# Kernel tuning notes

Measured on AMD Instinct MI355X. Metric: run time of the kernel, lower is better.

The kernel has to match this reference:

```python
import jax, jax.numpy as jnp
import numpy as np

N = 50000          # nodes
E = 1600000        # edges
H = 8              # heads
F = 16             # out feats per head (np1class)
IN = 256           # in feats
NEG_SLOPE = 0.2    # DGL GATConv default leaky_relu slope


def setup_inputs() -> dict:
    key = jax.random.key(0)
    ks = jax.random.split(key, 7)
    x = jax.random.normal(ks[0], (N, IN), dtype=jnp.float32)
    W = jax.random.normal(ks[1], (IN, H * F), dtype=jnp.float32) * 0.05
    attn_l = jax.random.normal(ks[2], (H, F), dtype=jnp.float32) * 0.05
    attn_r = jax.random.normal(ks[3], (H, F), dtype=jnp.float32) * 0.05
    bias = jax.random.normal(ks[4], (H * F,), dtype=jnp.float32) * 0.05
    src = jax.random.randint(ks[5], (E,), 0, N, dtype=jnp.int64)
    dst = jax.random.randint(ks[6], (E,), 0, N, dtype=jnp.int64)
    return {"x": x, "W": W, "attn_l": attn_l, "attn_r": attn_r,
            "bias": bias, "src": src, "dst": dst}


def reference(x, W, attn_l, attn_r, bias, src, dst):
    # Linear projection to heads: [N, H, F]
    feat = (x @ W).reshape(N, H, F)
    # Per-node attention halves: [N, H]
    el = jnp.einsum('nhf,hf->nh', feat, attn_l)
    er = jnp.einsum('nhf,hf->nh', feat, attn_r)
    # Edge scores: e = leaky_relu(el[src] + er[dst])  -> [E, H]
    e = jax.nn.leaky_relu(el[src] + er[dst], negative_slope=NEG_SLOPE)
    # Segment softmax over incoming edges of each destination node
    m = jax.ops.segment_max(e, dst, num_segments=N)           # [N, H]
    m = jnp.where(jnp.isfinite(m), m, 0.0)                    # empty segments
    m = jax.lax.stop_gradient(m)
    ex = jnp.exp(e - m[dst])                                  # [E, H]
    s = jax.ops.segment_sum(ex, dst, num_segments=N)          # [N, H]
    a = ex / jnp.maximum(s[dst], 1e-9)                        # [E, H]
    # Weighted aggregation of source features: [N, H, F]
    msg = a[:, :, None] * feat[src]
    rst = jax.ops.segment_sum(msg, dst, num_segments=N)
    rst = rst + bias.reshape(H, F)
    # Classifier: mean over heads -> [N, F]
    return rst.mean(axis=1)
```

## Files before the change

### kernel.cpp

```cpp
#include <hip/hip_runtime.h>
#include <hip/hip_bf16.h>

#define NH 8
#define NF 16
#define NIN 256
#define HF 128
#define BNODES 256
#define CAP 9216
#define BCH 4096

typedef __attribute__((ext_vector_type(8))) short bf16x8;
typedef __attribute__((ext_vector_type(4))) float f32x4;

__device__ __forceinline__ unsigned short f2bf(float f) {
    union { float f; unsigned int u; } v; v.f = f;
    unsigned int r = v.u + 0x7FFFu + ((v.u >> 16) & 1u);
    return (unsigned short)(r >> 16);
}
__device__ __forceinline__ float bf2f(unsigned short b) {
    union { unsigned int u; float f; } v; v.u = ((unsigned int)b) << 16;
    return v.f;
}

#define GROWS 128
__global__ __launch_bounds__(256) void gemm_mfma(const float* __restrict__ A,
                                                 const float* __restrict__ W,
                                                 const float* __restrict__ attn_l,
                                                 const float* __restrict__ attn_r,
                                                 unsigned short* __restrict__ featb,
                                                 float* __restrict__ el,
                                                 float* __restrict__ er, int M) {
    __shared__ unsigned short AsH[32][264];
    __shared__ unsigned short AsL[32][264];
    const int tid = threadIdx.x;
    const int wave = tid >> 6, lane = tid & 63;
    const int quad = lane >> 4, lq = lane & 15;
    const int row0 = blockIdx.x * GROWS;

    bf16x8 bfrag[8][2];
#pragma unroll
    for (int h2 = 0; h2 < 2; h2++) {
        const int col = (wave * 2 + h2) * 16 + lq;
#pragma unroll
        for (int kk = 0; kk < 8; kk++) {
            const int kb = kk * 32 + quad * 8;
            bf16x8 f;
#pragma unroll
            for (int j = 0; j < 8; j++)
                f[j] = (short)f2bf(W[(size_t)(kb + j) * HF + col]);
            bfrag[kk][h2] = f;
        }
    }
    const float al0 = attn_l[(wave * 2 + 0) * 16 + lq];
    const float al1 = attn_l[(wave * 2 + 1) * 16 + lq];
    const float ar0 = attn_r[(wave * 2 + 0) * 16 + lq];
    const float ar1 = attn_r[(wave * 2 + 1) * 16 + lq];

    const int srow = tid >> 3;

    for (int c = 0; c < 4; c++) {
        const int crow0 = row0 + c * 32;
        __syncthreads();
#pragma unroll
        for (int i = 0; i < 8; i++) {
            const int col = ((tid & 7) + i * 8) * 4;
            const int gr = crow0 + srow;
            float4 v = make_float4(0.f, 0.f, 0.f, 0.f);
            if (gr < M) v = *(const float4*)&A[(size_t)gr * NIN + col];
            const unsigned short h0 = f2bf(v.x), h1 = f2bf(v.y),
                                 h2b = f2bf(v.z), h3 = f2bf(v.w);
            *(ushort4*)&AsH[srow][col] = make_ushort4(h0, h1, h2b, h3);
            *(ushort4*)&AsL[srow][col] =
                make_ushort4(f2bf(v.x - bf2f(h0)), f2bf(v.y - bf2f(h1)),
                             f2bf(v.z - bf2f(h2b)), f2bf(v.w - bf2f(h3)));
        }
        __syncthreads();
#pragma unroll
        for (int s = 0; s < 2; s++) {
            f32x4 acc0 = {0.f, 0.f, 0.f, 0.f};
            f32x4 acc1 = {0.f, 0.f, 0.f, 0.f};
            const int ar = s * 16 + lq;
#pragma unroll
            for (int kk = 0; kk < 8; kk++) {
                const bf16x8 ah = *(const bf16x8*)&AsH[ar][kk * 32 + quad * 8];
                const bf16x8 al = *(const bf16x8*)&AsL[ar][kk * 32 + quad * 8];
                acc0 = __builtin_amdgcn_mfma_f32_16x16x32_bf16(ah, bfrag[kk][0], acc0, 0, 0, 0);
                acc1 = __builtin_amdgcn_mfma_f32_16x16x32_bf16(ah, bfrag[kk][1], acc1, 0, 0, 0);
                acc0 = __builtin_amdgcn_mfma_f32_16x16x32_bf16(al, bfrag[kk][0], acc0, 0, 0, 0);
                acc1 = __builtin_amdgcn_mfma_f32_16x16x32_bf16(al, bfrag[kk][1], acc1, 0, 0, 0);
            }
#pragma unroll
            for (int r = 0; r < 4; r++) {
                const int gr = crow0 + s * 16 + quad * 4 + r;
                float pl0 = acc0[r] * al0, pr0 = acc0[r] * ar0;
                float pl1 = acc1[r] * al1, pr1 = acc1[r] * ar1;
#pragma unroll
                for (int m = 1; m < 16; m <<= 1) {
                    pl0 += __shfl_xor(pl0, m, 64);
                    pr0 += __shfl_xor(pr0, m, 64);
                    pl1 += __shfl_xor(pl1, m, 64);
                    pr1 += __shfl_xor(pr1, m, 64);
                }
                if (gr < M) {
                    featb[(size_t)gr * HF + (wave * 2 + 0) * 16 + lq] = f2bf(acc0[r]);
                    featb[(size_t)gr * HF + (wave * 2 + 1) * 16 + lq] = f2bf(acc1[r]);
                    if (lq == 0) {
                        el[(size_t)gr * NH + wave * 2 + 0] = pl0;
                        el[(size_t)gr * NH + wave * 2 + 1] = pl1;
                        er[(size_t)gr * NH + wave * 2 + 0] = pr0;
                        er[(size_t)gr * NH + wave * 2 + 1] = pr1;
                    }
                }
            }
        }
    }
}

__global__ __launch_bounds__(256) void bin_kernel(const int* __restrict__ src,
                                                  const int* __restrict__ dst,
                                                  int* __restrict__ bcnt,
                                                  unsigned int* __restrict__ binned,
                                                  int E, int NB) {
    __shared__ unsigned int hist[256];
    __shared__ unsigned short lpos[BCH];
    const int tid = threadIdx.x;
    const int base = blockIdx.x * BCH;
    if (tid < NB) hist[tid] = 0;
    __syncthreads();
    const int cnt = min(BCH, E - base);
    for (int i = tid; i < cnt; i += 256) {
        const int b = dst[base + i] >> 8;
        lpos[i] = (unsigned short)atomicAdd(&hist[b], 1u);
    }
    __syncthreads();
    if (tid < NB) {
        const unsigned int c = hist[tid];
        if (c) hist[tid] = (unsigned int)(tid * CAP + atomicAdd(&bcnt[tid], (int)c));
    }
    __syncthreads();
    for (int i = tid; i < cnt; i += 256) {
        const int d = dst[base + i];
        const int b = d >> 8;
        const unsigned int pos = hist[b] + (unsigned int)lpos[i];
        binned[pos] = (unsigned int)src[base + i] | ((unsigned int)(d & 255) << 16);
    }
}

__global__ __launch_bounds__(256) void csr_kernel(const int* __restrict__ bcnt,
                                                  const unsigned int* __restrict__ binned,
                                                  int* __restrict__ nodeinfo,
                                                  unsigned short* __restrict__ srcsw,
                                                  int N) {
    __shared__ int len[BNODES], cur[BNODES];
    __shared__ int wsum[4];
    const int b = blockIdx.x, t = threadIdx.x;
    const int node0 = b << 8;
    const int cntb = bcnt[b];
    const unsigned int* bb = &binned[(size_t)b * CAP];
    unsigned short* sw = &srcsw[(size_t)b * CAP];
    len[t] = 0;
    __syncthreads();
    for (int i = t; i < cntb; i += 256) atomicAdd(&len[bb[i] >> 16], 1);
    __syncthreads();
    {
        const int lane = t & 63, w = t >> 6;
        const int v = len[t];
        int incl = v;
#pragma unroll
        for (int off = 1; off < 64; off <<= 1) {
            const int x = __shfl_up(incl, off, 64);
            if (lane >= off) incl += x;
        }
        if (lane == 63) wsum[w] = incl;
        __syncthreads();
        int wbase = 0;
        for (int k = 0; k < w; k++) wbase += wsum[k];
        const int excl = wbase + incl - v;
        cur[t] = excl;
        if (node0 + t < N) nodeinfo[node0 + t] = excl | (v << 16);
    }
    __syncthreads();
    for (int i = t; i < cntb; i += 256) {
        const unsigned int p = bb[i];
        const int pos = atomicAdd(&cur[p >> 16], 1);
        sw[pos] = (unsigned short)(p & 0xFFFFu);
    }
}

__global__ __launch_bounds__(128) void agg_kernel(const int* __restrict__ nodeinfo,
                                                  const unsigned short* __restrict__ srcsw,
                                                  const float* __restrict__ el,
                                                  const float* __restrict__ er,
                                                  const unsigned short* __restrict__ featb,
                                                  const float* __restrict__ bias,
                                                  float* __restrict__ out) {
    const int n = blockIdx.x;
    const int tid = threadIdx.x;
    __shared__ float lds_sc[32][8];
    __shared__ int lds_src[32];
    __shared__ float lds_ps[128];
    __shared__ float lds_s[8];
    __shared__ float2 lds_acc[2][64];
    __shared__ float2 lds_v[8][8];

    const int info = nodeinfo[n];
    const int begin = (n >> 8) * CAP + (info & 0xFFFF);
    const int end = begin + (info >> 16);
    const int hA = tid & 7, eA = tid >> 3;
    const float er_h = er[(size_t)n * NH + hA];
    const int w = tid >> 6, lane = tid & 63;
    const int hB = lane >> 3, fB2 = lane & 7;

    float2 acc = make_float2(0.f, 0.f);
    float psum = 0.f;
    for (int base = begin; base < end; base += 32) {
        const int cn = min(32, end - base);
#pragma unroll
        for (int rep = 0; rep < 2; rep++) {
            const int ei = eA + rep * 16;
            if (ei < cn) {
                const int si = (int)srcsw[base + ei];
                if (hA == 0) lds_src[ei] = si;
                float v = el[(size_t)si * NH + hA] + er_h;
                v = v > 0.f ? v : 0.2f * v;
                const float sc = __expf(v);
                lds_sc[ei][hA] = sc;
                psum += sc;
            }
        }
        __syncthreads();
        unsigned int fv[16];
#pragma unroll
        for (int j = 0; j < 16; j++) {
            const int ej = w * 16 + j;
            const int sj = lds_src[ej];
            fv[j] = (ej < cn)
                        ? *(const unsigned int*)&featb[(size_t)sj * HF + hB * 16 + fB2 * 2]
                        : 0u;
        }
#pragma unroll
        for (int j = 0; j < 16; j++) {
            const int ej = w * 16 + j;
            const float sc = (ej < cn) ? lds_sc[ej][hB] : 0.f;
            acc.x = fmaf(sc, bf2f((unsigned short)(fv[j] & 0xFFFFu)), acc.x);
            acc.y = fmaf(sc, bf2f((unsigned short)(fv[j] >> 16)), acc.y);
        }
        __syncthreads();
    }

    lds_ps[tid] = psum;
    lds_acc[w][lane] = acc;
    __syncthreads();
    if (tid < 8) {
        float s = 0.f;
#pragma unroll
        for (int k = 0; k < 16; k++) s += lds_ps[k * 8 + tid];
        lds_s[tid] = fmaxf(s, 1e-9f);
    }
    __syncthreads();
    if (tid < 64) {
        const float2 t0 = lds_acc[0][tid], t1 = lds_acc[1][tid];
        const float inv = 1.f / lds_s[hB];
        float2 val;
        val.x = (t0.x + t1.x) * inv + bias[hB * 16 + fB2 * 2];
        val.y = (t0.y + t1.y) * inv + bias[hB * 16 + fB2 * 2 + 1];
        lds_v[hB][fB2] = val;
    }
    __syncthreads();
    if (tid < 8) {
        float2 o = make_float2(0.f, 0.f);
#pragma unroll
        for (int h = 0; h < 8; h++) {
            const float2 v = lds_v[h][tid];
            o.x += v.x; o.y += v.y;
        }
        o.x *= 0.125f; o.y *= 0.125f;
        *(float2*)&out[(size_t)n * 16 + tid * 2] = o;
    }
}

extern "C" void kernel_launch(void* const* d_in, const int* in_sizes, int n_in,
                              void* d_out, int out_size, void* d_ws, size_t ws_size,
                              hipStream_t stream) {
    const float* x      = (const float*)d_in[0];
    const float* W      = (const float*)d_in[1];
    const float* attn_l = (const float*)d_in[2];
    const float* attn_r = (const float*)d_in[3];
    const float* bias   = (const float*)d_in[4];
    const int*   src    = (const int*)d_in[5];
    const int*   dst    = (const int*)d_in[6];
    float* out = (float*)d_out;

    const int N = in_sizes[0] / NIN;
    const int E = in_sizes[5];
    const int NB = (N + BNODES - 1) >> 8;

    char* w = (char*)d_ws;
    unsigned short* featb = (unsigned short*)w; w += (size_t)N * HF * 2;
    float* el     = (float*)w; w += (size_t)N * NH * 4;
    float* er     = (float*)w; w += (size_t)N * NH * 4;
    int* nodeinfo = (int*)w;   w += (size_t)N * 4;
    int* bcnt     = (int*)w;   w += (size_t)((NB + 15) & ~15) * 4;
    unsigned int* binned = (unsigned int*)w; w += (size_t)NB * CAP * 4;
    unsigned short* srcsw = (unsigned short*)w;

    hipMemsetAsync(bcnt, 0, (size_t)NB * sizeof(int), stream);

    gemm_mfma<<<(N + GROWS - 1) / GROWS, 256, 0, stream>>>(x, W, attn_l, attn_r,
                                                           featb, el, er, N);
    bin_kernel<<<(E + BCH - 1) / BCH, 256, 0, stream>>>(src, dst, bcnt, binned, E, NB);
    csr_kernel<<<NB, 256, 0, stream>>>(bcnt, binned, nodeinfo, srcsw, N);
    agg_kernel<<<N, 128, 0, stream>>>(nodeinfo, srcsw, el, er, featb, bias, out);
}
```

Baseline: 247.3 us.

## Bin edges locally per chunk with run table, stage CSR build in LDS

The binning kernel now sorts each 4096-edge chunk by destination bucket in shared memory and writes it out contiguously, recording each chunk's per-bucket offset and count in a run table. This replaces scattered global writes and the global atomic bucket counter, and drops the memset. The CSR kernel gathers its bucket's runs from every chunk into LDS, counts and scatters there, then writes srcsw back coalesced. The cost is more LDS per block, which limits occupancy, plus a serial prefix over the ~391 runs done by one thread and more small strided run reads.

```diff
diff --git a/kernel.cpp b/kernel.cpp
--- a/kernel.cpp
+++ b/kernel.cpp
@@ -118,52 +118,97 @@
 
 __global__ __launch_bounds__(256) void bin_kernel(const int* __restrict__ src,
                                                   const int* __restrict__ dst,
-                                                  int* __restrict__ bcnt,
                                                   unsigned int* __restrict__ binned,
-                                                  int E, int NB) {
+                                                  unsigned int* __restrict__ runtab,
+                                                  int E, int NB, int nbb) {
     __shared__ unsigned int hist[256];
+    __shared__ unsigned int offs[256];
+    __shared__ unsigned int wsum[4];
     __shared__ unsigned short lpos[BCH];
-    const int tid = threadIdx.x;
-    const int base = blockIdx.x * BCH;
-    if (tid < NB) hist[tid] = 0;
-    __syncthreads();
+    __shared__ unsigned int obuf[BCH];
+    const int blk = blockIdx.x, t = threadIdx.x;
+    const int base = blk * BCH;
     const int cnt = min(BCH, E - base);
-    for (int i = tid; i < cnt; i += 256) {
+    hist[t] = 0;
+    __syncthreads();
+    for (int i = t; i < cnt; i += 256) {
         const int b = dst[base + i] >> 8;
         lpos[i] = (unsigned short)atomicAdd(&hist[b], 1u);
     }
     __syncthreads();
-    if (tid < NB) {
-        const unsigned int c = hist[tid];
-        if (c) hist[tid] = (unsigned int)(tid * CAP + atomicAdd(&bcnt[tid], (int)c));
-    }
-    __syncthreads();
-    for (int i = tid; i < cnt; i += 256) {
+    {
+        const int lane = t & 63, w = t >> 6;
+        const unsigned int v = hist[t];
+        unsigned int incl = v;
+#pragma unroll
+        for (int off = 1; off < 64; off <<= 1) {
+            const unsigned int x = __shfl_up(incl, off, 64);
+            if (lane >= off) incl += x;
+        }
+        if (lane == 63) wsum[w] = incl;
+        __syncthreads();
+        unsigned int wbase = 0;
+        for (int k = 0; k < w; k++) wbase += wsum[k];
+        const unsigned int excl = wbase + incl - v;
+        offs[t] = excl;
+        if (t < NB) runtab[(size_t)t * nbb + blk] = excl | (v << 16);
+    }
+    __syncthreads();
+    for (int i = t; i < cnt; i += 256) {
         const int d = dst[base + i];
         const int b = d >> 8;
-        const unsigned int pos = hist[b] + (unsigned int)lpos[i];
-        binned[pos] = (unsigned int)src[base + i] | ((unsigned int)(d & 255) << 16);
-    }
-}
-
-__global__ __launch_bounds__(256) void csr_kernel(const int* __restrict__ bcnt,
-                                                  const unsigned int* __restrict__ binned,
+        obuf[offs[b] + lpos[i]] =
+            (unsigned int)src[base + i] | ((unsigned int)(d & 255) << 16);
+    }
+    __syncthreads();
+    for (int i = t; i < cnt; i += 256) binned[base + i] = obuf[i];
+}
+
+__global__ __launch_bounds__(256) void csr_kernel(const unsigned int* __restrict__ binned,
+                                                  const unsigned int* __restrict__ runtab,
                                                   int* __restrict__ nodeinfo,
                                                   unsigned short* __restrict__ srcsw,
-                                                  int N) {
+                                                  int N, int nbb) {
+    __shared__ unsigned int eary[CAP];
+    __shared__ unsigned short sSrc[CAP];
+    __shared__ unsigned int rinfo[512];
+    __shared__ unsigned short rcnt[512];
     __shared__ int len[BNODES], cur[BNODES];
     __shared__ int wsum[4];
+    __shared__ int tot_s;
     const int b = blockIdx.x, t = threadIdx.x;
     const int node0 = b << 8;
-    const int cntb = bcnt[b];
-    const unsigned int* bb = &binned[(size_t)b * CAP];
-    unsigned short* sw = &srcsw[(size_t)b * CAP];
+
+    for (int i = t; i < nbb; i += 256) {
+        const unsigned int e = runtab[(size_t)b * nbb + i];
+        rinfo[i] = e & 0xFFFFu;
+        rcnt[i] = (unsigned short)(e >> 16);
+    }
+    __syncthreads();
+    if (t == 0) {
+        unsigned int acc = 0;
+        for (int i = 0; i < nbb; i++) {
+            rinfo[i] |= acc << 16;
+            acc += rcnt[i];
+        }
+        tot_s = (int)acc;
+    }
+    __syncthreads();
+    const int tot = tot_s;
+    const int w = t >> 6, lane = t & 63;
+    for (int r = w; r < nbb; r += 4) {
+        const unsigned int inf = rinfo[r];
+        const int roff = (int)(inf & 0xFFFFu);
+        const int rbase = (int)(inf >> 16);
+        const int c = (int)rcnt[r];
+        for (int i = lane; i < c; i += 64)
+            eary[rbase + i] = binned[(size_t)r * BCH + roff + i];
+    }
     len[t] = 0;
     __syncthreads();
-    for (int i = t; i < cntb; i += 256) atomicAdd(&len[bb[i] >> 16], 1);
+    for (int i = t; i < tot; i += 256) atomicAdd(&len[eary[i] >> 16], 1);
     __syncthreads();
     {
-        const int lane = t & 63, w = t >> 6;
         const int v = len[t];
         int incl = v;
 #pragma unroll
@@ -180,11 +225,14 @@
         if (node0 + t < N) nodeinfo[node0 + t] = excl | (v << 16);
     }
     __syncthreads();
-    for (int i = t; i < cntb; i += 256) {
-        const unsigned int p = bb[i];
+    for (int i = t; i < tot; i += 256) {
+        const unsigned int p = eary[i];
         const int pos = atomicAdd(&cur[p >> 16], 1);
-        sw[pos] = (unsigned short)(p & 0xFFFFu);
-    }
+        sSrc[pos] = (unsigned short)(p & 0xFFFFu);
+    }
+    __syncthreads();
+    unsigned short* sw = &srcsw[(size_t)b * CAP];
+    for (int i = t; i < tot; i += 256) sw[i] = sSrc[i];
 }
 
 __global__ __launch_bounds__(128) void agg_kernel(const int* __restrict__ nodeinfo,
@@ -294,21 +342,20 @@
     const int N = in_sizes[0] / NIN;
     const int E = in_sizes[5];
     const int NB = (N + BNODES - 1) >> 8;
+    const int nbb = (E + BCH - 1) / BCH;
 
     char* w = (char*)d_ws;
     unsigned short* featb = (unsigned short*)w; w += (size_t)N * HF * 2;
     float* el     = (float*)w; w += (size_t)N * NH * 4;
     float* er     = (float*)w; w += (size_t)N * NH * 4;
     int* nodeinfo = (int*)w;   w += (size_t)N * 4;
-    int* bcnt     = (int*)w;   w += (size_t)((NB + 15) & ~15) * 4;
-    unsigned int* binned = (unsigned int*)w; w += (size_t)NB * CAP * 4;
+    unsigned int* binned = (unsigned int*)w; w += (size_t)nbb * BCH * 4;
+    unsigned int* runtab = (unsigned int*)w; w += (size_t)NB * nbb * 4;
     unsigned short* srcsw = (unsigned short*)w;
-
-    hipMemsetAsync(bcnt, 0, (size_t)NB * sizeof(int), stream);
 
     gemm_mfma<<<(N + GROWS - 1) / GROWS, 256, 0, stream>>>(x, W, attn_l, attn_r,
                                                            featb, el, er, N);
-    bin_kernel<<<(E + BCH - 1) / BCH, 256, 0, stream>>>(src, dst, bcnt, binned, E, NB);
-    csr_kernel<<<NB, 256, 0, stream>>>(bcnt, binned, nodeinfo, srcsw, N);
+    bin_kernel<<<nbb, 256, 0, stream>>>(src, dst, binned, runtab, E, NB, nbb);
+    csr_kernel<<<NB, 256, 0, stream>>>(binned, runtab, nodeinfo, srcsw, N, nbb);
     agg_kernel<<<N, 128, 0, stream>>>(nodeinfo, srcsw, el, er, featb, bias, out);
 }
```

Measured after the change: 266.5 us. +7.8%, slower.
